# Kernel tuning notes

Measured on AMD Instinct MI355X. Metric: run time of the kernel, lower is better.

The kernel has to match this reference:

```python
import jax, jax.numpy as jnp
import numpy as np

DIM = 512
HEADS = 8
HEAD_DIM = DIM // HEADS
SCALE = HEAD_DIM ** -0.5


def setup_inputs() -> dict:
    key = jax.random.key(0)
    ks = jax.random.split(key, 7)
    B, QN, N = 32, 128, 4096
    q = jax.random.normal(ks[0], (B, QN, DIM), dtype=jnp.float32)
    kv = jax.random.normal(ks[1], (B, N, DIM), dtype=jnp.float32)
    key_mask = jax.random.normal(ks[2], (B, QN, N), dtype=jnp.float32)
    Wq = jax.random.normal(ks[3], (DIM, DIM), dtype=jnp.float32) * 0.02
    Wkv = jax.random.normal(ks[4], (2 * DIM, DIM), dtype=jnp.float32) * 0.02
    Wproj = jax.random.normal(ks[5], (DIM, DIM), dtype=jnp.float32) * 0.02
    bproj = jax.random.normal(ks[6], (DIM,), dtype=jnp.float32) * 0.02
    return {"q": q, "kv": kv, "key_mask": key_mask,
            "Wq": Wq, "Wkv": Wkv, "Wproj": Wproj, "bproj": bproj}


def reference(q, kv, key_mask, Wq, Wkv, Wproj, bproj):
    B, QN, C = q.shape
    N = kv.shape[1]
    # q projection -> [B, QN, H, hd]
    qh = (q @ Wq.T).reshape(B, QN, HEADS, HEAD_DIM) * SCALE
    # kv projection -> split into k, v each [B, N, H, hd]
    kvp = kv @ Wkv.T  # [B, N, 2C]
    k = kvp[..., :C].reshape(B, N, HEADS, HEAD_DIM)
    v = kvp[..., C:].reshape(B, N, HEADS, HEAD_DIM)
    # scores [B, H, QN, N] + additive mask broadcast over heads
    attn = jnp.einsum('bqhd,bkhd->bhqk', qh, k) + key_mask[:, None]
    attn = jax.nn.softmax(attn, axis=-1)
    x = jnp.einsum('bhqk,bkhd->bqhd', attn, v).reshape(B, QN, C)
    return x @ Wproj.T + bproj
```

## Files before the change

### kernel.cpp

```cpp
#include <hip/hip_runtime.h>
#include <hip/hip_bf16.h>

typedef __attribute__((ext_vector_type(4))) float f32x4;
typedef __attribute__((ext_vector_type(8))) short bf16x8;
typedef __attribute__((ext_vector_type(4))) unsigned short ush4;

#define GAS __attribute__((address_space(1)))
#define LAS __attribute__((address_space(3)))

__device__ __forceinline__ unsigned int cvtpk(float lo, float hi) {
  unsigned int r;
  asm("v_cvt_pk_bf16_f32 %0, %1, %2" : "=v"(r) : "v"(lo), "v"(hi));
  return r;
}
__device__ __forceinline__ unsigned short f2bf(float f) { return (unsigned short)cvtpk(f, f); }
__device__ __forceinline__ f32x4 mfma16(bf16x8 a, bf16x8 b, f32x4 c) {
  return __builtin_amdgcn_mfma_f32_16x16x32_bf16(a, b, c, 0, 0, 0);
}
__device__ __forceinline__ void gl_lds16(const unsigned short* g, unsigned short* l) {
  __builtin_amdgcn_global_load_lds((const GAS unsigned short*)g, (LAS unsigned short*)l, 16, 0, 0);
}
__device__ __forceinline__ void memfence_sched() { asm volatile("" ::: "memory"); }

__global__ __launch_bounds__(256)
void cvt_f32_bf16(const float* __restrict__ in, unsigned short* __restrict__ out, int n8) {
  for (int i = blockIdx.x * blockDim.x + threadIdx.x; i < n8; i += gridDim.x * blockDim.x) {
    const float4 a = *reinterpret_cast<const float4*>(in + (size_t)i * 8);
    const float4 b = *reinterpret_cast<const float4*>(in + (size_t)i * 8 + 4);
    uint4 o;
    o.x = cvtpk(a.x, a.y); o.y = cvtpk(a.z, a.w);
    o.z = cvtpk(b.x, b.y); o.w = cvtpk(b.z, b.w);
    *reinterpret_cast<uint4*>(out + (size_t)i * 8) = o;
  }
}

template<int MODE, bool AF32, bool BF32>
__global__ __launch_bounds__(512, 2)
void gemm8(const void* __restrict__ Agv, const void* __restrict__ Bgv,
           void* __restrict__ Cg, void* __restrict__ Cg2,
           const float* __restrict__ bias, int ntn, size_t ldc)
{
  constexpr bool MIXED = AF32 || BF32;
  constexpr int NA = MIXED ? 2 : 3;
  constexpr int NB = MIXED ? 2 : 3;
  __shared__ unsigned short sm[(NA + NB) * 8192];
  unsigned short* const smB = sm + NA * 8192;

  const int t = threadIdx.x, lane = t & 63, w = t >> 6;
  const int lo = lane & 15, hi = lane >> 4;
  const int wm = w >> 2, wn = w & 3;
  const int nwg = gridDim.x, bid = blockIdx.x;
  const int id = (bid & 7) * (nwg >> 3) + (bid >> 3);
  const int row0 = (id / ntn) * 256, col0 = (id % ntn) * 256;
  const int w16 = w * 16;

  const unsigned short* Ab = (const unsigned short*)Agv;
  const unsigned short* Bb = (const unsigned short*)Bgv;
  const float* Ff = AF32 ? (const float*)Agv : (const float*)Bgv;
  const int frow0 = AF32 ? row0 : col0;

  const int cxor_g = (lane >> 3) & 3;
  const size_t a_src_g = (size_t)(row0 + w16 + (lane >> 2)) * 512 + (((lane & 3) ^ cxor_g) << 3);
  const size_t b_src_g = (size_t)(col0 + w16 + (lane >> 2)) * 512 + (((lane & 3) ^ cxor_g) << 3);

  const int rs_r = t >> 2;
  const int rs_c = (t & 3) * 8;
  const int wch = ((t & 3) ^ ((t >> 3) & 3)) << 3;

  float4 stF[2][4];

  auto F_ISSUE = [&](int kt) {
    if constexpr (MIXED) {
      const int bk = kt & 1;
      const float* s0 = Ff + (size_t)(frow0 + rs_r) * 512 + kt * 32 + rs_c;
      const float* s1 = Ff + (size_t)(frow0 + 128 + rs_r) * 512 + kt * 32 + rs_c;
      stF[bk][0] = *(const float4*)s0; stF[bk][1] = *(const float4*)(s0 + 4);
      stF[bk][2] = *(const float4*)s1; stF[bk][3] = *(const float4*)(s1 + 4);
    }
  };
  auto F_WRITE = [&](int kt) {
    if constexpr (MIXED) {
      const int bk = kt & 1;
      unsigned short* fb = AF32 ? &sm[(kt % NA) * 8192] : &smB[(kt % NB) * 8192];
      uint4 o;
      o.x = cvtpk(stF[bk][0].x, stF[bk][0].y); o.y = cvtpk(stF[bk][0].z, stF[bk][0].w);
      o.z = cvtpk(stF[bk][1].x, stF[bk][1].y); o.w = cvtpk(stF[bk][1].z, stF[bk][1].w);
      *reinterpret_cast<uint4*>(&fb[rs_r * 32 + wch]) = o;
      o.x = cvtpk(stF[bk][2].x, stF[bk][2].y); o.y = cvtpk(stF[bk][2].z, stF[bk][2].w);
      o.z = cvtpk(stF[bk][3].x, stF[bk][3].y); o.w = cvtpk(stF[bk][3].z, stF[bk][3].w);
      *reinterpret_cast<uint4*>(&fb[(128 + rs_r) * 32 + wch]) = o;
    }
  };
  auto G_ISSUE = [&](int kt) {
    if constexpr (!AF32) {
      unsigned short* ab = &sm[(kt % NA) * 8192];
      gl_lds16(Ab + a_src_g + kt * 32, ab + w16 * 32);
      gl_lds16(Ab + a_src_g + (size_t)128 * 512 + kt * 32, ab + (128 + w16) * 32);
    }
    if constexpr (!BF32) {
      unsigned short* bb = &smB[(kt % NB) * 8192];
      gl_lds16(Bb + b_src_g + kt * 32, bb + w16 * 32);
      gl_lds16(Bb + b_src_g + (size_t)128 * 512 + kt * 32, bb + (128 + w16) * 32);
    }
  };

  f32x4 acc[8][4] = {};
  const int fxor = (hi ^ ((lo >> 1) & 3)) << 3;

  if constexpr (MIXED) {
    F_ISSUE(0);
    G_ISSUE(0);
    F_ISSUE(1);
    memfence_sched();
    asm volatile("s_waitcnt vmcnt(6)" ::: "memory");
    F_WRITE(0);
    asm volatile("s_waitcnt vmcnt(4)" ::: "memory");
  } else {
    G_ISSUE(0); G_ISSUE(1);
    memfence_sched();
    asm volatile("s_waitcnt vmcnt(4)" ::: "memory");
  }
  asm volatile("s_waitcnt lgkmcnt(0)" ::: "memory");
  __builtin_amdgcn_s_barrier();
  memfence_sched();

  #pragma unroll
  for (int kt = 0; kt < 16; ++kt) {
    const unsigned short* ab = &sm[(kt % NA) * 8192];
    const unsigned short* bb = &smB[(kt % NB) * 8192];
    bf16x8 bfr[4], af[4];
    #pragma unroll
    for (int nj = 0; nj < 4; ++nj)
      bfr[nj] = *reinterpret_cast<const bf16x8*>(&bb[(wn * 64 + nj * 16 + lo) * 32 + fxor]);
    #pragma unroll
    for (int mi = 0; mi < 4; ++mi)
      af[mi] = *reinterpret_cast<const bf16x8*>(&ab[(wm * 128 + mi * 16 + lo) * 32 + fxor]);

    if constexpr (MIXED) {
      if (kt <= 14) G_ISSUE(kt + 1);
      if (kt <= 13) F_ISSUE(kt + 2);
    } else {
      if (kt <= 13) G_ISSUE(kt + 2);
    }
    memfence_sched();

    __builtin_amdgcn_s_setprio(1);
    #pragma unroll
    for (int mi = 0; mi < 4; ++mi)
      #pragma unroll
      for (int nj = 0; nj < 4; ++nj)
        acc[mi][nj] = mfma16(af[mi], bfr[nj], acc[mi][nj]);
    __builtin_amdgcn_s_setprio(0);

    #pragma unroll
    for (int mi = 0; mi < 4; ++mi)
      af[mi] = *reinterpret_cast<const bf16x8*>(&ab[(wm * 128 + (mi + 4) * 16 + lo) * 32 + fxor]);

    if constexpr (MIXED) {
      if (kt <= 13)      { asm volatile("s_waitcnt vmcnt(6)" ::: "memory"); }
      else if (kt == 14) { asm volatile("s_waitcnt vmcnt(2)" ::: "memory"); }
      if (kt <= 14) F_WRITE(kt + 1);
    }

    __builtin_amdgcn_s_setprio(1);
    #pragma unroll
    for (int mi = 0; mi < 4; ++mi)
      #pragma unroll
      for (int nj = 0; nj < 4; ++nj)
        acc[mi + 4][nj] = mfma16(af[mi], bfr[nj], acc[mi + 4][nj]);
    __builtin_amdgcn_s_setprio(0);

    if (kt < 15) {
      if (kt <= 13)      { asm volatile("s_waitcnt vmcnt(4)" ::: "memory"); }
      else               { asm volatile("s_waitcnt vmcnt(0)" ::: "memory"); }
      asm volatile("s_waitcnt lgkmcnt(0)" ::: "memory");
      __builtin_amdgcn_s_barrier();
      memfence_sched();
    }
  }

  if constexpr (MODE == 3) {
    __syncthreads();
    unsigned short* Tb = &sm[w * 4096];
    if (col0 < 512) {
      #pragma unroll
      for (int p = 0; p < 2; ++p) {
        #pragma unroll
        for (int q = 0; q < 4; ++q)
          #pragma unroll
          for (int nj = 0; nj < 4; ++nj)
            #pragma unroll
            for (int r = 0; r < 4; ++r)
              Tb[(q * 16 + hi * 4 + r) * 64 + nj * 16 + lo] = f2bf(acc[p * 4 + q][nj][r]);
        #pragma unroll
        for (int it = 0; it < 8; ++it) {
          const int rr = it * 8 + (lane >> 3);
          const bf16x8 v = *reinterpret_cast<const bf16x8*>(&Tb[rr * 64 + (lane & 7) * 8]);
          const size_t gm = (size_t)row0 + wm * 128 + p * 64 + rr;
          *reinterpret_cast<bf16x8*>((unsigned short*)Cg + gm * 512 + col0 + wn * 64 +
                                     (lane & 7) * 8) = v;
        }
      }
    } else {
      #pragma unroll
      for (int p = 0; p < 2; ++p) {
        #pragma unroll
        for (int q = 0; q < 4; ++q)
          #pragma unroll
          for (int nj = 0; nj < 4; ++nj)
            #pragma unroll
            for (int r = 0; r < 4; ++r) {
              const int gn_l = nj * 16 + lo;
              const int gm_l = (q * 16 + hi * 4 + r) ^ ((gn_l & 15) * 4);
              Tb[gn_l * 64 + gm_l] = f2bf(acc[p * 4 + q][nj][r]);
            }
        #pragma unroll
        for (int it = 0; it < 16; ++it) {
          const int gn_l = it * 4 + (lane >> 4);
          const int g4 = ((lane & 15) * 4) ^ ((gn_l & 15) * 4);
          const ush4 v = *reinterpret_cast<const ush4*>(&Tb[gn_l * 64 + g4]);
          const size_t vrow = (size_t)(col0 - 512) + wn * 64 + gn_l;
          const size_t vcol = (size_t)row0 + wm * 128 + p * 64 + (lane & 15) * 4;
          *reinterpret_cast<ush4*>((unsigned short*)Cg2 + vrow * 131072 + vcol) = v;
        }
      }
    }
  } else {
    #pragma unroll
    for (int mi = 0; mi < 8; ++mi) {
      #pragma unroll
      for (int r = 0; r < 4; ++r) {
        const size_t gm = (size_t)row0 + wm * 128 + mi * 16 + hi * 4 + r;
        #pragma unroll
        for (int nj = 0; nj < 4; ++nj) {
          const int gn = col0 + wn * 64 + nj * 16 + lo;
          const float v = acc[mi][nj][r];
          if constexpr (MODE == 0)
            ((unsigned short*)Cg)[gm * ldc + gn] = f2bf(v * 0.125f);
          else
            ((float*)Cg)[gm * ldc + gn] = v + bias[gn];
        }
      }
    }
  }
}

__global__ __launch_bounds__(256)
void attn_fwd(const unsigned short* __restrict__ qh,
              const unsigned short* __restrict__ kbuf,
              const unsigned short* __restrict__ vT,
              const float* __restrict__ mask,
              float* __restrict__ opart, float* __restrict__ ml)
{
  __shared__ unsigned short Ks[64 * 64];
  __shared__ unsigned short Vs[64 * 64];
  __shared__ unsigned short Ps[4][16 * 64];
  const int bid = blockIdx.x;
  const int xcd = bid & 7, g = bid >> 3;
  const int b = (g >> 6) * 8 + xcd;
  const int sub = g & 63;
  const int h = sub >> 3, qhalf = (sub >> 2) & 1, c = sub & 3;
  const int n0 = c * 1024;
  const int bh2 = (b * 8 + h) * 2 + qhalf;
  const int t = threadIdx.x, lane = t & 63, w = t >> 6;
  const int hi = lane >> 4, lo = lane & 15;
  const int q0 = qhalf * 64 + w * 16;

  bf16x8 aq[2];
  #pragma unroll
  for (int kk = 0; kk < 2; ++kk)
    aq[kk] = *reinterpret_cast<const bf16x8*>(
        qh + (size_t)(b * 128 + q0 + lo) * 512 + h * 64 + kk * 32 + hi * 8);

  float mrow[4], lrow[4];
  #pragma unroll
  for (int i = 0; i < 4; ++i) { mrow[i] = -1e30f; lrow[i] = 0.f; }
  f32x4 o[4] = {};

  const unsigned short* kp = kbuf + ((size_t)b * 4096 + n0) * 512 + h * 64;
  const unsigned short* vp = vT + (size_t)(h * 64) * 131072 + (size_t)b * 4096 + n0;
  const float* mp = mask + ((size_t)(b * 128 + q0)) * 4096 + n0;

  for (int nt = 0; nt < 16; ++nt) {
    {
      const int r = t >> 3, cc = t & 7;
      *reinterpret_cast<uint4*>(&Ks[r * 64 + ((cc ^ (r & 7)) << 3)]) =
          *reinterpret_cast<const uint4*>(kp + (size_t)(nt * 64 + r) * 512 + (cc << 3));
      *reinterpret_cast<uint4*>(&Ks[(r + 32) * 64 + ((cc ^ (r & 7)) << 3)]) =
          *reinterpret_cast<const uint4*>(kp + (size_t)(nt * 64 + r + 32) * 512 + (cc << 3));
      *reinterpret_cast<uint4*>(&Vs[r * 64 + ((cc ^ (r & 7)) << 3)]) =
          *reinterpret_cast<const uint4*>(vp + (size_t)r * 131072 + nt * 64 + (cc << 3));
      *reinterpret_cast<uint4*>(&Vs[(r + 32) * 64 + ((cc ^ (r & 7)) << 3)]) =
          *reinterpret_cast<const uint4*>(vp + (size_t)(r + 32) * 131072 + nt * 64 + (cc << 3));
    }
    __syncthreads();

    f32x4 s[4] = {};
    __builtin_amdgcn_s_setprio(1);
    #pragma unroll
    for (int ni = 0; ni < 4; ++ni) {
      #pragma unroll
      for (int kk = 0; kk < 2; ++kk) {
        const bf16x8 kf = *reinterpret_cast<const bf16x8*>(
            &Ks[(ni * 16 + lo) * 64 + ((kk * 32 + hi * 8) ^ ((lo & 7) << 3))]);
        s[ni] = mfma16(aq[kk], kf, s[ni]);
      }
    }
    __builtin_amdgcn_s_setprio(0);
    #pragma unroll
    for (int ni = 0; ni < 4; ++ni)
      #pragma unroll
      for (int r = 0; r < 4; ++r)
        s[ni][r] += mp[(size_t)(hi * 4 + r) * 4096 + nt * 64 + ni * 16 + lo];

    #pragma unroll
    for (int r = 0; r < 4; ++r) {
      float mx = fmaxf(fmaxf(s[0][r], s[1][r]), fmaxf(s[2][r], s[3][r]));
      #pragma unroll
      for (int off = 1; off < 16; off <<= 1)
        mx = fmaxf(mx, __shfl_xor(mx, off, 64));
      const float mnew = fmaxf(mrow[r], mx);
      const float corr = __expf(mrow[r] - mnew);
      mrow[r] = mnew;
      float ls = 0.f;
      #pragma unroll
      for (int ni = 0; ni < 4; ++ni) {
        const float p = __expf(s[ni][r] - mnew);
        s[ni][r] = p; ls += p;
      }
      #pragma unroll
      for (int off = 1; off < 16; off <<= 1)
        ls += __shfl_xor(ls, off, 64);
      lrow[r] = lrow[r] * corr + ls;
      #pragma unroll
      for (int di = 0; di < 4; ++di)
        o[di][r] *= corr;
    }

    #pragma unroll
    for (int ni = 0; ni < 4; ++ni)
      #pragma unroll
      for (int r = 0; r < 4; ++r) {
        const int rp = hi * 4 + r;
        Ps[w][rp * 64 + ((ni * 16 + lo) ^ ((rp & 7) << 3))] = f2bf(s[ni][r]);
      }

    __builtin_amdgcn_s_setprio(1);
    #pragma unroll
    for (int kk = 0; kk < 2; ++kk) {
      const bf16x8 pa = *reinterpret_cast<const bf16x8*>(
          &Ps[w][lo * 64 + ((kk * 32 + hi * 8) ^ ((lo & 7) << 3))]);
      #pragma unroll
      for (int di = 0; di < 4; ++di) {
        const bf16x8 vf = *reinterpret_cast<const bf16x8*>(
            &Vs[(di * 16 + lo) * 64 + ((kk * 32 + hi * 8) ^ ((lo & 7) << 3))]);
        o[di] = mfma16(pa, vf, o[di]);
      }
    }
    __builtin_amdgcn_s_setprio(0);
    __syncthreads();
  }

  const size_t pbase = ((size_t)bh2 * 4 + c) * 64;
  #pragma unroll
  for (int di = 0; di < 4; ++di)
    #pragma unroll
    for (int r = 0; r < 4; ++r)
      opart[(pbase + (w * 16 + hi * 4 + r)) * 64 + di * 16 + lo] = o[di][r];
  if (lo == 0) {
    #pragma unroll
    for (int r = 0; r < 4; ++r) {
      const int qq = w * 16 + hi * 4 + r;
      ml[(((size_t)bh2 * 4 + c) * 2 + 0) * 64 + qq] = mrow[r];
      ml[(((size_t)bh2 * 4 + c) * 2 + 1) * 64 + qq] = lrow[r];
    }
  }
}

__global__ __launch_bounds__(256)
void attn_combine(const float* __restrict__ opart, const float* __restrict__ ml,
                  unsigned short* __restrict__ xb)
{
  const int bh2 = blockIdx.x;
  const int b = bh2 >> 4, h = (bh2 >> 1) & 7, qhalf = bh2 & 1;
  const int t = threadIdx.x;
  const int q = t >> 2, dg = t & 3;

  float m[4], l[4];
  #pragma unroll
  for (int c = 0; c < 4; ++c) {
    m[c] = ml[(((size_t)bh2 * 4 + c) * 2 + 0) * 64 + q];
    l[c] = ml[(((size_t)bh2 * 4 + c) * 2 + 1) * 64 + q];
  }
  const float M = fmaxf(fmaxf(m[0], m[1]), fmaxf(m[2], m[3]));
  float sc[4], L = 0.f;
  #pragma unroll
  for (int c = 0; c < 4; ++c) { sc[c] = __expf(m[c] - M); L += sc[c] * l[c]; }
  const float inv = 1.f / L;

  float4 acc[4] = {};
  #pragma unroll
  for (int c = 0; c < 4; ++c) {
    const float* base = opart + (((size_t)bh2 * 4 + c) * 64 + q) * 64 + dg * 16;
    #pragma unroll
    for (int j = 0; j < 4; ++j) {
      const float4 v = *reinterpret_cast<const float4*>(base + j * 4);
      acc[j].x = fmaf(sc[c], v.x, acc[j].x);
      acc[j].y = fmaf(sc[c], v.y, acc[j].y);
      acc[j].z = fmaf(sc[c], v.z, acc[j].z);
      acc[j].w = fmaf(sc[c], v.w, acc[j].w);
    }
  }
  unsigned short* dst = xb + ((size_t)b * 128 + qhalf * 64 + q) * 512 + h * 64 + dg * 16;
  uint4 o1, o2;
  o1.x = cvtpk(acc[0].x * inv, acc[0].y * inv); o1.y = cvtpk(acc[0].z * inv, acc[0].w * inv);
  o1.z = cvtpk(acc[1].x * inv, acc[1].y * inv); o1.w = cvtpk(acc[1].z * inv, acc[1].w * inv);
  o2.x = cvtpk(acc[2].x * inv, acc[2].y * inv); o2.y = cvtpk(acc[2].z * inv, acc[2].w * inv);
  o2.z = cvtpk(acc[3].x * inv, acc[3].y * inv); o2.w = cvtpk(acc[3].z * inv, acc[3].w * inv);
  *reinterpret_cast<uint4*>(dst) = o1;
  *reinterpret_cast<uint4*>(dst + 8) = o2;
}

extern "C" void kernel_launch(void* const* d_in, const int* in_sizes, int n_in,
                              void* d_out, int out_size, void* d_ws, size_t ws_size,
                              hipStream_t stream) {
  const float* q     = (const float*)d_in[0];
  const float* kv    = (const float*)d_in[1];
  const float* mask  = (const float*)d_in[2];
  const float* Wq    = (const float*)d_in[3];
  const float* Wkv   = (const float*)d_in[4];
  const float* Wproj = (const float*)d_in[5];
  const float* bproj = (const float*)d_in[6];
  float* out = (float*)d_out;

  char* ws = (char*)d_ws;
  unsigned short* kbuf   = (unsigned short*)ws;
  unsigned short* vTb    = (unsigned short*)(ws + 134217728ULL);
  float*          opart  = (float*)(ws + 268435456ULL);
  float*          mlb    = (float*)(ws + 301989888ULL);
  unsigned short* qhb    = (unsigned short*)(ws + 303038464ULL);
  unsigned short* xb     = (unsigned short*)(ws + 307232768ULL);
  unsigned short* Wqb    = (unsigned short*)(ws + 311427072ULL);
  unsigned short* Wkvb   = (unsigned short*)(ws + 311951360ULL);
  unsigned short* Wprojb = (unsigned short*)(ws + 312999936ULL);

  cvt_f32_bf16<<<128, 256, 0, stream>>>(Wq, Wqb, 512 * 512 / 8);
  cvt_f32_bf16<<<256, 256, 0, stream>>>(Wkv, Wkvb, 1024 * 512 / 8);
  cvt_f32_bf16<<<128, 256, 0, stream>>>(Wproj, Wprojb, 512 * 512 / 8);

  gemm8<0, true, false><<<32, 512, 0, stream>>>(q, Wqb, qhb, nullptr, nullptr, 2, 512);
  gemm8<3, true, false><<<2048, 512, 0, stream>>>(kv, Wkvb, kbuf, vTb, nullptr, 4, 512);
  attn_fwd<<<2048, 256, 0, stream>>>(qhb, kbuf, vTb, mask, opart, mlb);
  attn_combine<<<512, 256, 0, stream>>>(opart, mlb, xb);
  gemm8<2, false, false><<<32, 512, 0, stream>>>(xb, Wprojb, out, nullptr, bproj, 2, 512);
}
```

Baseline: 432.0 us.

## Stage fp32 A tiles directly to LDS via async loads, convert at fragment read

The GEMM used for the q/kv projections now loads fp32 activation tiles straight into shared memory with global_load_lds and converts them to bf16 when each fragment is read. This replaces the earlier path that went through registers and converted before the shared-memory write. It also moves to a 3-slot ring buffer with one barrier per k-step and occupancy 1 (launch_bounds 512,1). The fp32 tile doubles the A shared-memory footprint and adds conversion work in the MFMA loop. Lower occupancy could expose latency in the large kv projection GEMM.

```diff
diff --git a/kernel.cpp b/kernel.cpp
--- a/kernel.cpp
+++ b/kernel.cpp
@@ -34,17 +34,16 @@
   }
 }
 
-template<int MODE, bool AF32, bool BF32>
-__global__ __launch_bounds__(512, 2)
-void gemm8(const void* __restrict__ Agv, const void* __restrict__ Bgv,
+template<int MODE, bool AF32>
+__global__ __launch_bounds__(512, 1)
+void gemmF(const void* __restrict__ Agv, const unsigned short* __restrict__ Bg,
            void* __restrict__ Cg, void* __restrict__ Cg2,
            const float* __restrict__ bias, int ntn, size_t ldc)
 {
-  constexpr bool MIXED = AF32 || BF32;
-  constexpr int NA = MIXED ? 2 : 3;
-  constexpr int NB = MIXED ? 2 : 3;
-  __shared__ unsigned short sm[(NA + NB) * 8192];
-  unsigned short* const smB = sm + NA * 8192;
+  constexpr int ASLOT = AF32 ? 16384 : 8192;
+  constexpr int LPT = AF32 ? 6 : 4;
+  __shared__ unsigned short sm[3 * ASLOT + 3 * 8192];
+  unsigned short* const smB = sm + 3 * ASLOT;
 
   const int t = threadIdx.x, lane = t & 63, w = t >> 6;
   const int lo = lane & 15, hi = lane >> 4;
@@ -52,131 +51,120 @@
   const int nwg = gridDim.x, bid = blockIdx.x;
   const int id = (bid & 7) * (nwg >> 3) + (bid >> 3);
   const int row0 = (id / ntn) * 256, col0 = (id % ntn) * 256;
-  const int w16 = w * 16;
-
+
+  const float* Af = (const float*)Agv;
   const unsigned short* Ab = (const unsigned short*)Agv;
-  const unsigned short* Bb = (const unsigned short*)Bgv;
-  const float* Ff = AF32 ? (const float*)Agv : (const float*)Bgv;
-  const int frow0 = AF32 ? row0 : col0;
-
-  const int cxor_g = (lane >> 3) & 3;
-  const size_t a_src_g = (size_t)(row0 + w16 + (lane >> 2)) * 512 + (((lane & 3) ^ cxor_g) << 3);
-  const size_t b_src_g = (size_t)(col0 + w16 + (lane >> 2)) * 512 + (((lane & 3) ^ cxor_g) << 3);
-
-  const int rs_r = t >> 2;
-  const int rs_c = (t & 3) * 8;
-  const int wch = ((t & 3) ^ ((t >> 3) & 3)) << 3;
-
-  float4 stF[2][4];
-
-  auto F_ISSUE = [&](int kt) {
-    if constexpr (MIXED) {
-      const int bk = kt & 1;
-      const float* s0 = Ff + (size_t)(frow0 + rs_r) * 512 + kt * 32 + rs_c;
-      const float* s1 = Ff + (size_t)(frow0 + 128 + rs_r) * 512 + kt * 32 + rs_c;
-      stF[bk][0] = *(const float4*)s0; stF[bk][1] = *(const float4*)(s0 + 4);
-      stF[bk][2] = *(const float4*)s1; stF[bk][3] = *(const float4*)(s1 + 4);
+
+  const int ar8 = t >> 3;
+  const int ac8 = ((t & 7) ^ (ar8 & 7)) * 4;
+  const int ar4 = t >> 2;
+  const int ac4 = ((t & 3) ^ (ar4 & 3)) * 8;
+  const unsigned short* bS = Bg + (size_t)(col0 + ar4) * 512 + ac4;
+
+  auto STAGE_A = [&](int kt) {
+    if constexpr (AF32) {
+      unsigned short* dst = &sm[(kt % 3) * 16384 + w * 512];
+      const float* src = Af + (size_t)(row0 + ar8) * 512 + kt * 32 + ac8;
+      #pragma unroll
+      for (int i = 0; i < 4; ++i)
+        gl_lds16((const unsigned short*)(src + (size_t)i * 64 * 512), dst + i * 4096);
+    } else {
+      unsigned short* dst = &sm[(kt % 3) * 8192 + w * 512];
+      const unsigned short* src = Ab + (size_t)(row0 + ar4) * 512 + kt * 32 + ac4;
+      gl_lds16(src, dst);
+      gl_lds16(src + (size_t)128 * 512, dst + 4096);
     }
   };
-  auto F_WRITE = [&](int kt) {
-    if constexpr (MIXED) {
-      const int bk = kt & 1;
-      unsigned short* fb = AF32 ? &sm[(kt % NA) * 8192] : &smB[(kt % NB) * 8192];
-      uint4 o;
-      o.x = cvtpk(stF[bk][0].x, stF[bk][0].y); o.y = cvtpk(stF[bk][0].z, stF[bk][0].w);
-      o.z = cvtpk(stF[bk][1].x, stF[bk][1].y); o.w = cvtpk(stF[bk][1].z, stF[bk][1].w);
-      *reinterpret_cast<uint4*>(&fb[rs_r * 32 + wch]) = o;
-      o.x = cvtpk(stF[bk][2].x, stF[bk][2].y); o.y = cvtpk(stF[bk][2].z, stF[bk][2].w);
-      o.z = cvtpk(stF[bk][3].x, stF[bk][3].y); o.w = cvtpk(stF[bk][3].z, stF[bk][3].w);
-      *reinterpret_cast<uint4*>(&fb[(128 + rs_r) * 32 + wch]) = o;
-    }
+  auto STAGE_B = [&](int kt) {
+    unsigned short* dst = &smB[(kt % 3) * 8192 + w * 512];
+    gl_lds16(bS + kt * 32, dst);
+    gl_lds16(bS + (size_t)128 * 512 + kt * 32, dst + 4096);
   };
-  auto G_ISSUE = [&](int kt) {
-    if constexpr (!AF32) {
-      unsigned short* ab = &sm[(kt % NA) * 8192];
-      gl_lds16(Ab + a_src_g + kt * 32, ab + w16 * 32);
-      gl_lds16(Ab + a_src_g + (size_t)128 * 512 + kt * 32, ab + (128 + w16) * 32);
-    }
-    if constexpr (!BF32) {
-      unsigned short* bb = &smB[(kt % NB) * 8192];
-      gl_lds16(Bb + b_src_g + kt * 32, bb + w16 * 32);
-      gl_lds16(Bb + b_src_g + (size_t)128 * 512 + kt * 32, bb + (128 + w16) * 32);
-    }
-  };
 
   f32x4 acc[8][4] = {};
-  const int fxor = (hi ^ ((lo >> 1) & 3)) << 3;
-
-  if constexpr (MIXED) {
-    F_ISSUE(0);
-    G_ISSUE(0);
-    F_ISSUE(1);
-    memfence_sched();
-    asm volatile("s_waitcnt vmcnt(6)" ::: "memory");
-    F_WRITE(0);
-    asm volatile("s_waitcnt vmcnt(4)" ::: "memory");
-  } else {
-    G_ISSUE(0); G_ISSUE(1);
-    memfence_sched();
-    asm volatile("s_waitcnt vmcnt(4)" ::: "memory");
-  }
-  asm volatile("s_waitcnt lgkmcnt(0)" ::: "memory");
+
+  STAGE_A(0); STAGE_B(0); STAGE_A(1); STAGE_B(1);
+  memfence_sched();
+  if constexpr (AF32) asm volatile("s_waitcnt vmcnt(6)" ::: "memory");
+  else                asm volatile("s_waitcnt vmcnt(4)" ::: "memory");
   __builtin_amdgcn_s_barrier();
   memfence_sched();
 
   #pragma unroll
   for (int kt = 0; kt < 16; ++kt) {
-    const unsigned short* ab = &sm[(kt % NA) * 8192];
-    const unsigned short* bb = &smB[(kt % NB) * 8192];
-    bf16x8 bfr[4], af[4];
-    #pragma unroll
-    for (int nj = 0; nj < 4; ++nj)
-      bfr[nj] = *reinterpret_cast<const bf16x8*>(&bb[(wn * 64 + nj * 16 + lo) * 32 + fxor]);
+    if (kt <= 13) { STAGE_A(kt + 2); STAGE_B(kt + 2); }
+    memfence_sched();
+
+    const unsigned short* aB = &sm[(kt % 3) * ASLOT];
+    const unsigned short* bB = &smB[(kt % 3) * 8192];
+
+    bf16x8 bfr[4], a0[4], a1[4];
+    #pragma unroll
+    for (int nj = 0; nj < 4; ++nj) {
+      const int r = wn * 64 + nj * 16 + lo;
+      bfr[nj] = *reinterpret_cast<const bf16x8*>(&bB[r * 32 + ((hi ^ (lo & 3)) * 8)]);
+    }
+    if constexpr (AF32) {
+      const float* afp = (const float*)aB;
+      #pragma unroll
+      for (int mi = 0; mi < 4; ++mi) {
+        const int r = wm * 128 + mi * 16 + lo;
+        const float4 p = *reinterpret_cast<const float4*>(
+            afp + r * 32 + (((2 * hi)     ^ (lo & 7)) * 4));
+        const float4 q = *reinterpret_cast<const float4*>(
+            afp + r * 32 + (((2 * hi + 1) ^ (lo & 7)) * 4));
+        uint4 u;
+        u.x = cvtpk(p.x, p.y); u.y = cvtpk(p.z, p.w);
+        u.z = cvtpk(q.x, q.y); u.w = cvtpk(q.z, q.w);
+        a0[mi] = __builtin_bit_cast(bf16x8, u);
+      }
+      #pragma unroll
+      for (int mi = 0; mi < 4; ++mi) {
+        const int r = wm * 128 + (mi + 4) * 16 + lo;
+        const float4 p = *reinterpret_cast<const float4*>(
+            afp + r * 32 + (((2 * hi)     ^ (lo & 7)) * 4));
+        const float4 q = *reinterpret_cast<const float4*>(
+            afp + r * 32 + (((2 * hi + 1) ^ (lo & 7)) * 4));
+        uint4 u;
+        u.x = cvtpk(p.x, p.y); u.y = cvtpk(p.z, p.w);
+        u.z = cvtpk(q.x, q.y); u.w = cvtpk(q.z, q.w);
+        a1[mi] = __builtin_bit_cast(bf16x8, u);
+      }
+    } else {
+      #pragma unroll
+      for (int mi = 0; mi < 4; ++mi) {
+        const int r = wm * 128 + mi * 16 + lo;
+        a0[mi] = *reinterpret_cast<const bf16x8*>(&aB[r * 32 + ((hi ^ (lo & 3)) * 8)]);
+      }
+      #pragma unroll
+      for (int mi = 0; mi < 4; ++mi) {
+        const int r = wm * 128 + (mi + 4) * 16 + lo;
+        a1[mi] = *reinterpret_cast<const bf16x8*>(&aB[r * 32 + ((hi ^ (lo & 3)) * 8)]);
+      }
+    }
+    asm volatile("s_waitcnt lgkmcnt(0)" ::: "memory");
+    __builtin_amdgcn_sched_barrier(0);
+
+    __builtin_amdgcn_s_setprio(1);
     #pragma unroll
     for (int mi = 0; mi < 4; ++mi)
-      af[mi] = *reinterpret_cast<const bf16x8*>(&ab[(wm * 128 + mi * 16 + lo) * 32 + fxor]);
-
-    if constexpr (MIXED) {
-      if (kt <= 14) G_ISSUE(kt + 1);
-      if (kt <= 13) F_ISSUE(kt + 2);
-    } else {
-      if (kt <= 13) G_ISSUE(kt + 2);
-    }
-    memfence_sched();
-
-    __builtin_amdgcn_s_setprio(1);
+      #pragma unroll
+      for (int nj = 0; nj < 4; ++nj)
+        acc[mi][nj] = mfma16(a0[mi], bfr[nj], acc[mi][nj]);
     #pragma unroll
     for (int mi = 0; mi < 4; ++mi)
       #pragma unroll
       for (int nj = 0; nj < 4; ++nj)
-        acc[mi][nj] = mfma16(af[mi], bfr[nj], acc[mi][nj]);
+        acc[mi + 4][nj] = mfma16(a1[mi], bfr[nj], acc[mi + 4][nj]);
     __builtin_amdgcn_s_setprio(0);
 
-    #pragma unroll
-    for (int mi = 0; mi < 4; ++mi)
-      af[mi] = *reinterpret_cast<const bf16x8*>(&ab[(wm * 128 + (mi + 4) * 16 + lo) * 32 + fxor]);
-
-    if constexpr (MIXED) {
-      if (kt <= 13)      { asm volatile("s_waitcnt vmcnt(6)" ::: "memory"); }
-      else if (kt == 14) { asm volatile("s_waitcnt vmcnt(2)" ::: "memory"); }
-      if (kt <= 14) F_WRITE(kt + 1);
-    }
-
-    __builtin_amdgcn_s_setprio(1);
-    #pragma unroll
-    for (int mi = 0; mi < 4; ++mi)
-      #pragma unroll
-      for (int nj = 0; nj < 4; ++nj)
-        acc[mi + 4][nj] = mfma16(af[mi], bfr[nj], acc[mi + 4][nj]);
-    __builtin_amdgcn_s_setprio(0);
-
-    if (kt < 15) {
-      if (kt <= 13)      { asm volatile("s_waitcnt vmcnt(4)" ::: "memory"); }
-      else               { asm volatile("s_waitcnt vmcnt(0)" ::: "memory"); }
-      asm volatile("s_waitcnt lgkmcnt(0)" ::: "memory");
-      __builtin_amdgcn_s_barrier();
-      memfence_sched();
-    }
+    if (kt <= 13) {
+      if constexpr (AF32) asm volatile("s_waitcnt vmcnt(6)" ::: "memory");
+      else                asm volatile("s_waitcnt vmcnt(4)" ::: "memory");
+    } else if (kt == 14) {
+      asm volatile("s_waitcnt vmcnt(0)" ::: "memory");
+    }
+    if (kt < 15) { __builtin_amdgcn_s_barrier(); memfence_sched(); }
   }
 
   if constexpr (MODE == 3) {
@@ -192,6 +180,7 @@
             #pragma unroll
             for (int r = 0; r < 4; ++r)
               Tb[(q * 16 + hi * 4 + r) * 64 + nj * 16 + lo] = f2bf(acc[p * 4 + q][nj][r]);
+        asm volatile("s_waitcnt lgkmcnt(0)" ::: "memory");
         #pragma unroll
         for (int it = 0; it < 8; ++it) {
           const int rr = it * 8 + (lane >> 3);
@@ -214,6 +203,7 @@
               const int gm_l = (q * 16 + hi * 4 + r) ^ ((gn_l & 15) * 4);
               Tb[gn_l * 64 + gm_l] = f2bf(acc[p * 4 + q][nj][r]);
             }
+        asm volatile("s_waitcnt lgkmcnt(0)" ::: "memory");
         #pragma unroll
         for (int it = 0; it < 16; ++it) {
           const int gn_l = it * 4 + (lane >> 4);
@@ -223,6 +213,7 @@
           const size_t vcol = (size_t)row0 + wm * 128 + p * 64 + (lane & 15) * 4;
           *reinterpret_cast<ush4*>((unsigned short*)Cg2 + vrow * 131072 + vcol) = v;
         }
+        __builtin_amdgcn_s_barrier();
       }
     }
   } else {
@@ -448,9 +439,9 @@
   cvt_f32_bf16<<<256, 256, 0, stream>>>(Wkv, Wkvb, 1024 * 512 / 8);
   cvt_f32_bf16<<<128, 256, 0, stream>>>(Wproj, Wprojb, 512 * 512 / 8);
 
-  gemm8<0, true, false><<<32, 512, 0, stream>>>(q, Wqb, qhb, nullptr, nullptr, 2, 512);
-  gemm8<3, true, false><<<2048, 512, 0, stream>>>(kv, Wkvb, kbuf, vTb, nullptr, 4, 512);
+  gemmF<0, true><<<32, 512, 0, stream>>>(q, Wqb, qhb, nullptr, nullptr, 2, 512);
+  gemmF<3, true><<<2048, 512, 0, stream>>>(kv, Wkvb, kbuf, vTb, nullptr, 4, 512);
   attn_fwd<<<2048, 256, 0, stream>>>(qhb, kbuf, vTb, mask, opart, mlb);
   attn_combine<<<512, 256, 0, stream>>>(opart, mlb, xb);
-  gemm8<2, false, false><<<32, 512, 0, stream>>>(xb, Wprojb, out, nullptr, bproj, 2, 512);
-}
+  gemmF<2, false><<<32, 512, 0, stream>>>(xb, Wprojb, out, nullptr, bproj, 2, 512);
+}
```

New measurement: 489.5 us. 1.13x slower.

## Shrink projection GEMM tiles to 128x128 with 256-thread blocks

Applied to the files above, without the earlier changes.

Replaces the 256x256, 512-thread GEMM with a 128x128, 256-thread variant using double-buffered LDS and targeting three blocks per CU. Grid sizes for the q, kv and output projections grow fourfold, which gives the small q and output GEMMs far more blocks across the CUs. The cost is lower data reuse per tile, so more global and LDS traffic for the large kv projection. The bf16-only path also drops its deeper prefetch and now waits on all loads every k-step.

```diff
diff --git a/kernel.cpp b/kernel.cpp
--- a/kernel.cpp
+++ b/kernel.cpp
@@ -34,80 +34,72 @@
   }
 }
 
-template<int MODE, bool AF32, bool BF32>
-__global__ __launch_bounds__(512, 2)
-void gemm8(const void* __restrict__ Agv, const void* __restrict__ Bgv,
+template<int MODE, bool AF32>
+__global__ __launch_bounds__(256, 3)
+void gemmM(const void* __restrict__ Agv, const unsigned short* __restrict__ Bg,
            void* __restrict__ Cg, void* __restrict__ Cg2,
            const float* __restrict__ bias, int ntn, size_t ldc)
 {
-  constexpr bool MIXED = AF32 || BF32;
-  constexpr int NA = MIXED ? 2 : 3;
-  constexpr int NB = MIXED ? 2 : 3;
-  __shared__ unsigned short sm[(NA + NB) * 8192];
-  unsigned short* const smB = sm + NA * 8192;
+  __shared__ unsigned short sm[16384];
+  unsigned short* const smB = sm + 8192;
 
   const int t = threadIdx.x, lane = t & 63, w = t >> 6;
   const int lo = lane & 15, hi = lane >> 4;
-  const int wm = w >> 2, wn = w & 3;
+  const int wm = w >> 1, wn = w & 1;
   const int nwg = gridDim.x, bid = blockIdx.x;
   const int id = (bid & 7) * (nwg >> 3) + (bid >> 3);
-  const int row0 = (id / ntn) * 256, col0 = (id % ntn) * 256;
-  const int w16 = w * 16;
-
+  const int row0 = (id / ntn) * 128, col0 = (id % ntn) * 128;
+
+  const float* Af = (const float*)Agv;
   const unsigned short* Ab = (const unsigned short*)Agv;
-  const unsigned short* Bb = (const unsigned short*)Bgv;
-  const float* Ff = AF32 ? (const float*)Agv : (const float*)Bgv;
-  const int frow0 = AF32 ? row0 : col0;
-
-  const int cxor_g = (lane >> 3) & 3;
-  const size_t a_src_g = (size_t)(row0 + w16 + (lane >> 2)) * 512 + (((lane & 3) ^ cxor_g) << 3);
-  const size_t b_src_g = (size_t)(col0 + w16 + (lane >> 2)) * 512 + (((lane & 3) ^ cxor_g) << 3);
+
+  const int swcol = ((lane & 3) ^ ((lane >> 3) & 3)) * 8;
+  const unsigned short* bS = Bg + (size_t)(col0 + w * 32 + (lane >> 2)) * 512 + swcol;
+  const unsigned short* aSg = Ab + (size_t)(row0 + w * 32 + (lane >> 2)) * 512 + swcol;
 
   const int rs_r = t >> 2;
   const int rs_c = (t & 3) * 8;
-  const int wch = ((t & 3) ^ ((t >> 3) & 3)) << 3;
+  const int wch = ((t & 3) ^ ((t >> 3) & 3)) * 8;
 
   float4 stF[2][4];
 
   auto F_ISSUE = [&](int kt) {
-    if constexpr (MIXED) {
+    if constexpr (AF32) {
       const int bk = kt & 1;
-      const float* s0 = Ff + (size_t)(frow0 + rs_r) * 512 + kt * 32 + rs_c;
-      const float* s1 = Ff + (size_t)(frow0 + 128 + rs_r) * 512 + kt * 32 + rs_c;
+      const float* s0 = Af + (size_t)(row0 + rs_r) * 512 + kt * 32 + rs_c;
+      const float* s1 = Af + (size_t)(row0 + 64 + rs_r) * 512 + kt * 32 + rs_c;
       stF[bk][0] = *(const float4*)s0; stF[bk][1] = *(const float4*)(s0 + 4);
       stF[bk][2] = *(const float4*)s1; stF[bk][3] = *(const float4*)(s1 + 4);
     }
   };
   auto F_WRITE = [&](int kt) {
-    if constexpr (MIXED) {
+    if constexpr (AF32) {
       const int bk = kt & 1;
-      unsigned short* fb = AF32 ? &sm[(kt % NA) * 8192] : &smB[(kt % NB) * 8192];
+      unsigned short* fb = &sm[(kt & 1) * 4096];
       uint4 o;
       o.x = cvtpk(stF[bk][0].x, stF[bk][0].y); o.y = cvtpk(stF[bk][0].z, stF[bk][0].w);
       o.z = cvtpk(stF[bk][1].x, stF[bk][1].y); o.w = cvtpk(stF[bk][1].z, stF[bk][1].w);
       *reinterpret_cast<uint4*>(&fb[rs_r * 32 + wch]) = o;
       o.x = cvtpk(stF[bk][2].x, stF[bk][2].y); o.y = cvtpk(stF[bk][2].z, stF[bk][2].w);
       o.z = cvtpk(stF[bk][3].x, stF[bk][3].y); o.w = cvtpk(stF[bk][3].z, stF[bk][3].w);
-      *reinterpret_cast<uint4*>(&fb[(128 + rs_r) * 32 + wch]) = o;
+      *reinterpret_cast<uint4*>(&fb[(64 + rs_r) * 32 + wch]) = o;
     }
   };
   auto G_ISSUE = [&](int kt) {
+    unsigned short* bb = &smB[(kt & 1) * 4096];
+    gl_lds16(bS + kt * 32,                     bb + (w * 2 + 0) * 512);
+    gl_lds16(bS + (size_t)16 * 512 + kt * 32,  bb + (w * 2 + 1) * 512);
     if constexpr (!AF32) {
-      unsigned short* ab = &sm[(kt % NA) * 8192];
-      gl_lds16(Ab + a_src_g + kt * 32, ab + w16 * 32);
-      gl_lds16(Ab + a_src_g + (size_t)128 * 512 + kt * 32, ab + (128 + w16) * 32);
-    }
-    if constexpr (!BF32) {
-      unsigned short* bb = &smB[(kt % NB) * 8192];
-      gl_lds16(Bb + b_src_g + kt * 32, bb + w16 * 32);
-      gl_lds16(Bb + b_src_g + (size_t)128 * 512 + kt * 32, bb + (128 + w16) * 32);
+      unsigned short* ab = &sm[(kt & 1) * 4096];
+      gl_lds16(aSg + kt * 32,                    ab + (w * 2 + 0) * 512);
+      gl_lds16(aSg + (size_t)16 * 512 + kt * 32, ab + (w * 2 + 1) * 512);
     }
   };
 
-  f32x4 acc[8][4] = {};
-  const int fxor = (hi ^ ((lo >> 1) & 3)) << 3;
-
-  if constexpr (MIXED) {
+  f32x4 acc[4][4] = {};
+  const int fxor = (hi ^ ((lo >> 1) & 3)) * 8;
+
+  if constexpr (AF32) {
     F_ISSUE(0);
     G_ISSUE(0);
     F_ISSUE(1);
@@ -116,9 +108,9 @@
     F_WRITE(0);
     asm volatile("s_waitcnt vmcnt(4)" ::: "memory");
   } else {
-    G_ISSUE(0); G_ISSUE(1);
+    G_ISSUE(0);
     memfence_sched();
-    asm volatile("s_waitcnt vmcnt(4)" ::: "memory");
+    asm volatile("s_waitcnt vmcnt(0)" ::: "memory");
   }
   asm volatile("s_waitcnt lgkmcnt(0)" ::: "memory");
   __builtin_amdgcn_s_barrier();
@@ -126,37 +118,29 @@
 
   #pragma unroll
   for (int kt = 0; kt < 16; ++kt) {
-    const unsigned short* ab = &sm[(kt % NA) * 8192];
-    const unsigned short* bb = &smB[(kt % NB) * 8192];
+    const unsigned short* ab = &sm[(kt & 1) * 4096];
+    const unsigned short* bb = &smB[(kt & 1) * 4096];
     bf16x8 bfr[4], af[4];
     #pragma unroll
     for (int nj = 0; nj < 4; ++nj)
       bfr[nj] = *reinterpret_cast<const bf16x8*>(&bb[(wn * 64 + nj * 16 + lo) * 32 + fxor]);
     #pragma unroll
     for (int mi = 0; mi < 4; ++mi)
-      af[mi] = *reinterpret_cast<const bf16x8*>(&ab[(wm * 128 + mi * 16 + lo) * 32 + fxor]);
-
-    if constexpr (MIXED) {
-      if (kt <= 14) G_ISSUE(kt + 1);
-      if (kt <= 13) F_ISSUE(kt + 2);
-    } else {
-      if (kt <= 13) G_ISSUE(kt + 2);
-    }
+      af[mi] = *reinterpret_cast<const bf16x8*>(&ab[(wm * 64 + mi * 16 + lo) * 32 + fxor]);
+
+    if (kt <= 14) G_ISSUE(kt + 1);
+    if constexpr (AF32) { if (kt <= 13) F_ISSUE(kt + 2); }
     memfence_sched();
 
     __builtin_amdgcn_s_setprio(1);
     #pragma unroll
-    for (int mi = 0; mi < 4; ++mi)
+    for (int mi = 0; mi < 2; ++mi)
       #pragma unroll
       for (int nj = 0; nj < 4; ++nj)
         acc[mi][nj] = mfma16(af[mi], bfr[nj], acc[mi][nj]);
     __builtin_amdgcn_s_setprio(0);
 
-    #pragma unroll
-    for (int mi = 0; mi < 4; ++mi)
-      af[mi] = *reinterpret_cast<const bf16x8*>(&ab[(wm * 128 + (mi + 4) * 16 + lo) * 32 + fxor]);
-
-    if constexpr (MIXED) {
+    if constexpr (AF32) {
       if (kt <= 13)      { asm volatile("s_waitcnt vmcnt(6)" ::: "memory"); }
       else if (kt == 14) { asm volatile("s_waitcnt vmcnt(2)" ::: "memory"); }
       if (kt <= 14) F_WRITE(kt + 1);
@@ -164,15 +148,19 @@
 
     __builtin_amdgcn_s_setprio(1);
     #pragma unroll
-    for (int mi = 0; mi < 4; ++mi)
+    for (int mi = 2; mi < 4; ++mi)
       #pragma unroll
       for (int nj = 0; nj < 4; ++nj)
-        acc[mi + 4][nj] = mfma16(af[mi], bfr[nj], acc[mi + 4][nj]);
+        acc[mi][nj] = mfma16(af[mi], bfr[nj], acc[mi][nj]);
     __builtin_amdgcn_s_setprio(0);
 
     if (kt < 15) {
-      if (kt <= 13)      { asm volatile("s_waitcnt vmcnt(4)" ::: "memory"); }
-      else               { asm volatile("s_waitcnt vmcnt(0)" ::: "memory"); }
+      if constexpr (AF32) {
+        if (kt <= 13) { asm volatile("s_waitcnt vmcnt(4)" ::: "memory"); }
+        else          { asm volatile("s_waitcnt vmcnt(0)" ::: "memory"); }
+      } else {
+        asm volatile("s_waitcnt vmcnt(0)" ::: "memory");
+      }
       asm volatile("s_waitcnt lgkmcnt(0)" ::: "memory");
       __builtin_amdgcn_s_barrier();
       memfence_sched();
@@ -184,53 +172,49 @@
     unsigned short* Tb = &sm[w * 4096];
     if (col0 < 512) {
       #pragma unroll
-      for (int p = 0; p < 2; ++p) {
+      for (int q = 0; q < 4; ++q)
         #pragma unroll
-        for (int q = 0; q < 4; ++q)
+        for (int nj = 0; nj < 4; ++nj)
           #pragma unroll
-          for (int nj = 0; nj < 4; ++nj)
-            #pragma unroll
-            for (int r = 0; r < 4; ++r)
-              Tb[(q * 16 + hi * 4 + r) * 64 + nj * 16 + lo] = f2bf(acc[p * 4 + q][nj][r]);
+          for (int r = 0; r < 4; ++r)
+            Tb[(q * 16 + hi * 4 + r) * 64 + nj * 16 + lo] = f2bf(acc[q][nj][r]);
+      asm volatile("s_waitcnt lgkmcnt(0)" ::: "memory");
+      #pragma unroll
+      for (int it = 0; it < 8; ++it) {
+        const int rr = it * 8 + (lane >> 3);
+        const bf16x8 v = *reinterpret_cast<const bf16x8*>(&Tb[rr * 64 + (lane & 7) * 8]);
+        const size_t gm = (size_t)row0 + wm * 64 + rr;
+        *reinterpret_cast<bf16x8*>((unsigned short*)Cg + gm * 512 + col0 + wn * 64 +
+                                   (lane & 7) * 8) = v;
+      }
+    } else {
+      #pragma unroll
+      for (int q = 0; q < 4; ++q)
         #pragma unroll
-        for (int it = 0; it < 8; ++it) {
-          const int rr = it * 8 + (lane >> 3);
-          const bf16x8 v = *reinterpret_cast<const bf16x8*>(&Tb[rr * 64 + (lane & 7) * 8]);
-          const size_t gm = (size_t)row0 + wm * 128 + p * 64 + rr;
-          *reinterpret_cast<bf16x8*>((unsigned short*)Cg + gm * 512 + col0 + wn * 64 +
-                                     (lane & 7) * 8) = v;
-        }
-      }
-    } else {
-      #pragma unroll
-      for (int p = 0; p < 2; ++p) {
-        #pragma unroll
-        for (int q = 0; q < 4; ++q)
+        for (int nj = 0; nj < 4; ++nj)
           #pragma unroll
-          for (int nj = 0; nj < 4; ++nj)
-            #pragma unroll
-            for (int r = 0; r < 4; ++r) {
-              const int gn_l = nj * 16 + lo;
-              const int gm_l = (q * 16 + hi * 4 + r) ^ ((gn_l & 15) * 4);
-              Tb[gn_l * 64 + gm_l] = f2bf(acc[p * 4 + q][nj][r]);
-            }
-        #pragma unroll
-        for (int it = 0; it < 16; ++it) {
-          const int gn_l = it * 4 + (lane >> 4);
-          const int g4 = ((lane & 15) * 4) ^ ((gn_l & 15) * 4);
-          const ush4 v = *reinterpret_cast<const ush4*>(&Tb[gn_l * 64 + g4]);
-          const size_t vrow = (size_t)(col0 - 512) + wn * 64 + gn_l;
-          const size_t vcol = (size_t)row0 + wm * 128 + p * 64 + (lane & 15) * 4;
-          *reinterpret_cast<ush4*>((unsigned short*)Cg2 + vrow * 131072 + vcol) = v;
-        }
+          for (int r = 0; r < 4; ++r) {
+            const int gn_l = nj * 16 + lo;
+            const int gm_l = (q * 16 + hi * 4 + r) ^ ((gn_l & 15) * 4);
+            Tb[gn_l * 64 + gm_l] = f2bf(acc[q][nj][r]);
+          }
+      asm volatile("s_waitcnt lgkmcnt(0)" ::: "memory");
+      #pragma unroll
+      for (int it = 0; it < 16; ++it) {
+        const int gn_l = it * 4 + (lane >> 4);
+        const int g4 = ((lane & 15) * 4) ^ ((gn_l & 15) * 4);
+        const ush4 v = *reinterpret_cast<const ush4*>(&Tb[gn_l * 64 + g4]);
+        const size_t vrow = (size_t)(col0 - 512) + wn * 64 + gn_l;
+        const size_t vcol = (size_t)row0 + wm * 64 + (lane & 15) * 4;
+        *reinterpret_cast<ush4*>((unsigned short*)Cg2 + vrow * 131072 + vcol) = v;
       }
     }
   } else {
     #pragma unroll
-    for (int mi = 0; mi < 8; ++mi) {
+    for (int mi = 0; mi < 4; ++mi) {
       #pragma unroll
       for (int r = 0; r < 4; ++r) {
-        const size_t gm = (size_t)row0 + wm * 128 + mi * 16 + hi * 4 + r;
+        const size_t gm = (size_t)row0 + wm * 64 + mi * 16 + hi * 4 + r;
         #pragma unroll
         for (int nj = 0; nj < 4; ++nj) {
           const int gn = col0 + wn * 64 + nj * 16 + lo;
@@ -448,9 +432,9 @@
   cvt_f32_bf16<<<256, 256, 0, stream>>>(Wkv, Wkvb, 1024 * 512 / 8);
   cvt_f32_bf16<<<128, 256, 0, stream>>>(Wproj, Wprojb, 512 * 512 / 8);
 
-  gemm8<0, true, false><<<32, 512, 0, stream>>>(q, Wqb, qhb, nullptr, nullptr, 2, 512);
-  gemm8<3, true, false><<<2048, 512, 0, stream>>>(kv, Wkvb, kbuf, vTb, nullptr, 4, 512);
+  gemmM<0, true><<<128, 256, 0, stream>>>(q, Wqb, qhb, nullptr, nullptr, 4, 512);
+  gemmM<3, true><<<8192, 256, 0, stream>>>(kv, Wkvb, kbuf, vTb, nullptr, 8, 512);
   attn_fwd<<<2048, 256, 0, stream>>>(qhb, kbuf, vTb, mask, opart, mlb);
   attn_combine<<<512, 256, 0, stream>>>(opart, mlb, xb);
-  gemm8<2, false, false><<<32, 512, 0, stream>>>(xb, Wprojb, out, nullptr, bproj, 2, 512);
-}
+  gemmM<2, false><<<128, 256, 0, stream>>>(xb, Wprojb, out, nullptr, bproj, 4, 512);
+}
```

Result: faster. 420.4 us (-2.7%).
